# Optimization experiments

Hardware: AMD Instinct MI355X
Metric: run time of the kernel (lower is better)

The kernel has to match this reference:

```python
import jax, jax.numpy as jnp
import numpy as np

H = 2048   # hidden_size
NH = 32    # n_head
HS = 64    # head_size
B, T = 2, 4096
D_DECAY, D_AAA, D_MV, D_GATE = 96, 96, 64, 256


def setup_inputs() -> dict:
    key = jax.random.key(0)
    ks = jax.random.split(key, 30)
    rn = lambda k, s, sc=0.02: jax.random.normal(k, s, jnp.float32) * sc
    d = {}
    d['x'] = jax.random.normal(ks[0], (B, T, H), jnp.float32)
    d['shift_state_in'] = jax.random.normal(ks[1], (B, H), jnp.float32)
    d['wkv_state_in'] = jnp.zeros((B, NH, HS, HS), jnp.float32)
    d['v_first_val'] = jax.random.normal(ks[2], (B, T, H), jnp.float32)
    for i, n in enumerate(['x_r', 'x_w', 'x_k', 'x_v', 'x_a', 'x_g']):
        d[n] = jax.random.uniform(ks[3 + i], (H,), jnp.float32)
    d['w0'] = rn(ks[9], (H,)) - 4.0
    d['w1'] = rn(ks[10], (H, D_DECAY)); d['w2'] = rn(ks[11], (D_DECAY, H))
    d['a0'] = rn(ks[12], (H,)); d['a1'] = rn(ks[13], (H, D_AAA)); d['a2'] = rn(ks[14], (D_AAA, H))
    d['v0'] = rn(ks[15], (H,)) + 1.0; d['v1'] = rn(ks[16], (H, D_MV)); d['v2'] = rn(ks[17], (D_MV, H))
    d['g1'] = rn(ks[18], (H, D_GATE)); d['g2'] = rn(ks[19], (D_GATE, H))
    d['k_k'] = jnp.full((H,), 0.85, jnp.float32)
    d['k_a'] = jnp.ones((H,), jnp.float32)
    d['r_k'] = rn(ks[20], (NH, HS))
    s = 1.0 / np.sqrt(H)
    d['W_r'] = jax.random.normal(ks[21], (H, H), jnp.float32) * s
    d['W_k'] = jax.random.normal(ks[22], (H, H), jnp.float32) * s
    d['W_v'] = jax.random.normal(ks[23], (H, H), jnp.float32) * s
    d['W_o'] = jax.random.normal(ks[24], (H, H), jnp.float32) * s
    d['ln_w'] = jnp.ones((H,), jnp.float32)
    d['ln_b'] = jnp.zeros((H,), jnp.float32)
    return d


def _forward(x, shift_state_in, wkv_state_in, v_first_val, x_r, x_w, x_k, x_v, x_a, x_g,
             w0, w1, w2, a0, a1, a2, v0, v1, v2, g1, g2, k_k, k_a, r_k,
             W_r, W_k, W_v, W_o, ln_w, ln_b):
    Bx, Tx, C = x.shape
    # token shift: previous token embedding (shift_state for t=0)
    xprev = jnp.concatenate([shift_state_in[:, None, :], x[:, :-1]], axis=1)
    dx = xprev - x
    xr, xw, xk, xv, xa, xg = (x + dx * m for m in (x_r, x_w, x_k, x_v, x_a, x_g))
    r = xr @ W_r.T
    k = xk @ W_k.T
    v = xv @ W_v.T
    # soft-clamped log-decay (<= -0.5)
    w_raw = -jax.nn.softplus(-(w0 + jnp.tanh(xw @ w1) @ w2)) - 0.5
    # layer_id > 0: residual mix with first-layer value
    v = v + (v_first_val - v) * jax.nn.sigmoid(v0 + (xv @ v1) @ v2)
    a = jax.nn.sigmoid(a0 + (xa @ a1) @ a2)          # in-context learning rate
    g = jax.nn.sigmoid(xg @ g1) @ g2                 # output gate
    kk = (k * k_k).reshape(Bx, Tx, NH, HS)
    kk = kk / jnp.maximum(jnp.linalg.norm(kk, axis=-1, keepdims=True), 1e-12)  # F.normalize
    kk = kk.reshape(Bx, Tx, C)
    k = k * (1.0 + (a - 1.0) * k_a)
    w = jnp.exp(-jnp.exp(w_raw))                     # per-channel decay in (0,1)
    heads = lambda t: t.reshape(Bx, Tx, NH, HS).transpose(1, 0, 2, 3)  # [T,B,NH,HS]
    rs, ws, ks_, vs, kks, as_ = map(heads, (r, w, k, v, kk, a))

    def step(S, inp):
        # S: [B,NH,HS(value),HS(key)]
        rt, wt, kt, vt, kkt, at = inp
        sa = jnp.einsum('bhvk,bhk->bhv', S, -kkt)
        S = (S * wt[:, :, None, :]
             + sa[:, :, :, None] * (kkt * at)[:, :, None, :]
             + vt[:, :, :, None] * kt[:, :, None, :])
        return S, jnp.einsum('bhvk,bhk->bhv', S, rt)

    wkv_state_out, y = jax.lax.scan(step, wkv_state_in, (rs, ws, ks_, vs, kks, as_))
    y = y.transpose(1, 0, 2, 3)                      # [B,T,NH,HS]
    # GroupNorm(n_head groups, eps=1e-5*head_size)
    mu = y.mean(-1, keepdims=True)
    var = y.var(-1, keepdims=True)
    y = ((y - mu) / jnp.sqrt(var + 1e-5 * HS)).reshape(Bx, Tx, C) * ln_w + ln_b
    rk = (r.reshape(Bx, Tx, NH, HS) * k.reshape(Bx, Tx, NH, HS) * r_k).sum(-1, keepdims=True)
    y = y + (rk * v.reshape(Bx, Tx, NH, HS)).reshape(Bx, Tx, C)
    out = (y * g) @ W_o.T
    return out, x[:, -1], wkv_state_out, v_first_val


def reference(x, shift_state_in, wkv_state_in, v_first_val, x_r, x_w, x_k, x_v, x_a, x_g,
              w0, w1, w2, a0, a1, a2, v0, v1, v2, g1, g2, k_k, k_a, r_k,
              W_r, W_k, W_v, W_o, ln_w, ln_b):
    return _forward(x, shift_state_in, wkv_state_in, v_first_val, x_r, x_w, x_k, x_v, x_a, x_g,
                    w0, w1, w2, a0, a1, a2, v0, v1, v2, g1, g2, k_k, k_a, r_k,
                    W_r, W_k, W_v, W_o, ln_w, ln_b)
```

## Files before the change

### kernel.cpp

```cpp
#include <hip/hip_runtime.h>

typedef unsigned short u16;
typedef __attribute__((ext_vector_type(4))) float f32x4;
typedef __attribute__((ext_vector_type(8))) __bf16 bf16x8;
typedef __attribute__((ext_vector_type(8))) unsigned short u16x8;
typedef __attribute__((ext_vector_type(4))) unsigned short u16x4;

#define DI static __device__ __forceinline__

DI float bfu2f(u16 u){ unsigned int x = ((unsigned int)u)<<16; float f; __builtin_memcpy(&f,&x,4); return f; }
DI u16 f2bfu(float f){ __bf16 h = (__bf16)f; u16 u; __builtin_memcpy(&u,&h,2); return u; }
DI float sigm(float x){ return 1.f/(1.f+expf(-x)); }

DI void gload_lds16(const void* g, void* l) {
  __builtin_amdgcn_global_load_lds(
      (const __attribute__((address_space(1))) unsigned int*)g,
      (__attribute__((address_space(3))) unsigned int*)l, 16, 0, 0);
}

template<bool OBF16>
__global__ __launch_bounds__(256) void gemm128_k(
    const u16* __restrict__ A, const u16* __restrict__ Bt,
    void* __restrict__ Cp, int M, int N, int K)
{
  __shared__ alignas(16) u16 As[128*64];
  __shared__ alignas(16) u16 Bs[128*64];
  const int tid = threadIdx.x;
  const int wid = tid >> 6, lane = tid & 63;
  const int wm = wid >> 1, wn = wid & 1;
  const int l15 = lane & 15, q = lane >> 4;
  const int m0 = blockIdx.x * 128, n0 = blockIdx.y * 128;
  const int sr = (wid << 3) + (lane >> 3);
  const int sc = (lane & 7) << 3;
  f32x4 acc[4][4];
  #pragma unroll
  for (int i=0;i<4;i++)
    #pragma unroll
    for (int j=0;j<4;j++) acc[i][j] = f32x4{0.f,0.f,0.f,0.f};

  char* la = (char*)As + (size_t)wid*1024;
  char* lb = (char*)Bs + (size_t)wid*1024;
  for (int k0 = 0; k0 < K; k0 += 64) {
    const u16* ga = A  + (size_t)(m0 + sr)*K + k0 + sc;
    const u16* gb = Bt + (size_t)(n0 + sr)*K + k0 + sc;
    #pragma unroll
    for (int it = 0; it < 4; ++it) {
      gload_lds16(ga + (size_t)(32*it)*K, la + it*4096);
      gload_lds16(gb + (size_t)(32*it)*K, lb + it*4096);
    }
    __syncthreads();
    #pragma unroll
    for (int ks = 0; ks < 64; ks += 32) {
      bf16x8 af[4], bfv[4];
      #pragma unroll
      for (int i=0;i<4;i++) af[i]  = *(const bf16x8*)&As[(wm*64 + i*16 + l15)*64 + ks + q*8];
      #pragma unroll
      for (int j=0;j<4;j++) bfv[j] = *(const bf16x8*)&Bs[(wn*64 + j*16 + l15)*64 + ks + q*8];
      #pragma unroll
      for (int i=0;i<4;i++)
        #pragma unroll
        for (int j=0;j<4;j++)
          acc[i][j] = __builtin_amdgcn_mfma_f32_16x16x32_bf16(af[i], bfv[j], acc[i][j], 0, 0, 0);
    }
    __syncthreads();
  }
  #pragma unroll
  for (int i=0;i<4;i++)
    #pragma unroll
    for (int j=0;j<4;j++)
      #pragma unroll
      for (int rr=0;rr<4;rr++) {
        const int gm = m0 + wm*64 + i*16 + q*4 + rr;
        const int gn = n0 + wn*64 + j*16 + l15;
        const size_t o = (size_t)gm * (size_t)N + gn;
        if constexpr (OBF16) ((u16*)Cp)[o] = f2bfu(acc[i][j][rr]);
        else                 ((float*)Cp)[o] = acc[i][j][rr];
      }
}

constexpr int LDW = 72;

template<bool MIX, bool WNK, bool ABF16, bool OBF16, int EPI=0>
__global__ __launch_bounds__(256) void gemm_k(
    const void* __restrict__ Ap, const float* __restrict__ dxp, const float* __restrict__ mixp,
    const float* __restrict__ Wp, void* __restrict__ Cp, int M, int N, int K)
{
  __shared__ alignas(16) __bf16 As[64*LDW];
  __shared__ alignas(16) __bf16 Bs[64*LDW];
  const int tid = threadIdx.x;
  const int m0 = blockIdx.x * 64;
  const int n0 = blockIdx.y * 64;
  const int lane = tid & 63, wid = tid >> 6;
  const int wm = wid >> 1, wn = wid & 1;
  const int l15 = lane & 15, q = lane >> 4;
  f32x4 acc[2][2] = {{{0.f,0.f,0.f,0.f},{0.f,0.f,0.f,0.f}},
                     {{0.f,0.f,0.f,0.f},{0.f,0.f,0.f,0.f}}};

  for (int k0 = 0; k0 < K; k0 += 64) {
    {
      const int kc = (tid & 7) * 8;
      const int r0 = tid >> 3;
      #pragma unroll
      for (int it = 0; it < 2; ++it) {
        const int row = r0 + 32*it;
        const size_t gmK = (size_t)(m0 + row) * (size_t)K;
        const int gk = k0 + kc;
        if constexpr (ABF16) {
          const u16* A16 = (const u16*)Ap;
          u16x8 u;
          if (gk + 7 < K) u = *(const u16x8*)(A16 + gmK + gk);
          else {
            #pragma unroll
            for (int e=0;e<8;e++) u[e] = (gk+e < K) ? A16[gmK + gk + e] : (u16)0;
          }
          *(u16x8*)&As[row*LDW + kc] = u;
        } else {
          const float* A32 = (const float*)Ap;
          float f[8];
          if (gk + 7 < K) {
            f32x4 va = *(const f32x4*)(A32 + gmK + gk);
            f32x4 vb = *(const f32x4*)(A32 + gmK + gk + 4);
            if constexpr (MIX) {
              f32x4 d0 = *(const f32x4*)(dxp + gmK + gk);
              f32x4 d1 = *(const f32x4*)(dxp + gmK + gk + 4);
              f32x4 c0 = *(const f32x4*)(mixp + gk);
              f32x4 c1 = *(const f32x4*)(mixp + gk + 4);
              va = va + d0*c0; vb = vb + d1*c1;
            }
            #pragma unroll
            for (int e=0;e<4;e++){ f[e]=va[e]; f[4+e]=vb[e]; }
          } else {
            #pragma unroll
            for (int e=0;e<8;e++){
              const int kk2 = gk+e;
              float xv = 0.f;
              if (kk2 < K) {
                xv = A32[gmK + kk2];
                if constexpr (MIX) xv = fmaf(dxp[gmK+kk2], mixp[kk2], xv);
              }
              f[e] = xv;
            }
          }
          bf16x8 v8;
          #pragma unroll
          for (int e=0;e<8;e++) v8[e] = (__bf16)f[e];
          *(bf16x8*)&As[row*LDW + kc] = v8;
        }
      }
    }
    if constexpr (WNK) {
      const int kc = (tid & 7) * 8;
      const int r0 = tid >> 3;
      #pragma unroll
      for (int it = 0; it < 2; ++it) {
        const int row = r0 + 32*it;
        const int gn = n0 + row;
        const int gk = k0 + kc;
        float f[8];
        if (gn < N && gk + 7 < K) {
          const size_t o = (size_t)gn * (size_t)K + gk;
          f32x4 va = *(const f32x4*)(Wp + o);
          f32x4 vb = *(const f32x4*)(Wp + o + 4);
          #pragma unroll
          for (int e=0;e<4;e++){ f[e]=va[e]; f[4+e]=vb[e]; }
        } else {
          #pragma unroll
          for (int e=0;e<8;e++) f[e] = (gn < N && gk+e < K) ? Wp[(size_t)gn*K + gk + e] : 0.f;
        }
        bf16x8 v8;
        #pragma unroll
        for (int e=0;e<8;e++) v8[e] = (__bf16)f[e];
        *(bf16x8*)&Bs[row*LDW + kc] = v8;
      }
    } else {
      const int nc = (tid & 15) * 4;
      const int kr = tid >> 4;
      #pragma unroll
      for (int it = 0; it < 4; ++it) {
        const int kk = kr + 16*it;
        const int gk = k0 + kk;
        f32x4 v = {0.f,0.f,0.f,0.f};
        if (gk < K) {
          const int gn = n0 + nc;
          if (gn + 3 < N) v = *(const f32x4*)(Wp + (size_t)gk*N + gn);
          else {
            #pragma unroll
            for (int e=0;e<4;e++) if (gn+e < N) v[e] = Wp[(size_t)gk*N + gn + e];
          }
        }
        #pragma unroll
        for (int e=0;e<4;e++) Bs[(nc+e)*LDW + kk] = (__bf16)v[e];
      }
    }
    __syncthreads();
    #pragma unroll
    for (int ks = 0; ks < 64; ks += 32) {
      bf16x8 af[2], bfv[2];
      #pragma unroll
      for (int i=0;i<2;i++) af[i]  = *(const bf16x8*)&As[(wm*32 + i*16 + l15)*LDW + ks + q*8];
      #pragma unroll
      for (int i=0;i<2;i++) bfv[i] = *(const bf16x8*)&Bs[(wn*32 + i*16 + l15)*LDW + ks + q*8];
      #pragma unroll
      for (int i=0;i<2;i++)
        #pragma unroll
        for (int j=0;j<2;j++)
          acc[i][j] = __builtin_amdgcn_mfma_f32_16x16x32_bf16(af[i], bfv[j], acc[i][j], 0, 0, 0);
    }
    __syncthreads();
  }
  #pragma unroll
  for (int i=0;i<2;i++) {
    #pragma unroll
    for (int j=0;j<2;j++) {
      #pragma unroll
      for (int rr=0;rr<4;rr++) {
        const int gm = m0 + wm*32 + i*16 + q*4 + rr;
        const int gn = n0 + wn*32 + j*16 + l15;
        if (gn < N) {
          const size_t o = (size_t)gm * (size_t)N + gn;
          if constexpr (EPI == 1) {
            float* C = (float*)Cp;
            const float s = sigm(mixp[gn] + acc[i][j][rr]);
            const float vG = C[o];
            C[o] = vG + (dxp[o] - vG) * s;
          } else if constexpr (OBF16) {
            ((u16*)Cp)[o] = f2bfu(acc[i][j][rr]);
          } else {
            ((float*)Cp)[o] = acc[i][j][rr];
          }
        }
      }
    }
  }
}

__global__ void mix_cast_k(const float* __restrict__ x, const float* __restrict__ shift,
    const float* __restrict__ mr, const float* __restrict__ mw, const float* __restrict__ mk,
    const float* __restrict__ mv, const float* __restrict__ ma, const float* __restrict__ mg,
    u16* __restrict__ xr_b, u16* __restrict__ xw_b, u16* __restrict__ xk_b,
    u16* __restrict__ xv_b, u16* __restrict__ xa_b, u16* __restrict__ xg_b,
    float* __restrict__ xlast, int T_, int B_)
{
  const int Hh = 2048;
  size_t e4 = (size_t)blockIdx.x*blockDim.x + threadIdx.x;
  size_t total4 = (size_t)B_*T_*Hh/4;
  if (e4 >= total4) return;
  size_t e = e4*4;
  size_t th = (size_t)T_*Hh;
  size_t b = e / th; size_t rem = e - b*th;
  int t = (int)(rem / Hh); int c = (int)(rem & (Hh-1));
  f32x4 xv4 = *(const f32x4*)(x+e);
  f32x4 xp = t ? *(const f32x4*)(x+e-Hh) : *(const f32x4*)(shift + b*Hh + c);
  f32x4 dx = xp - xv4;
  if (t == T_-1) *(f32x4*)(xlast + b*Hh + c) = xv4;
  #define EMIT(mp, dst) { \
    f32x4 mc = *(const f32x4*)(mp + c); \
    f32x4 r_ = xv4 + dx*mc; \
    u16x4 o_; \
    o_[0]=f2bfu(r_[0]); o_[1]=f2bfu(r_[1]); o_[2]=f2bfu(r_[2]); o_[3]=f2bfu(r_[3]); \
    *(u16x4*)(dst + e) = o_; }
  EMIT(mr, xr_b) EMIT(mw, xw_b) EMIT(mk, xk_b)
  EMIT(mv, xv_b) EMIT(ma, xa_b) EMIT(mg, xg_b)
  #undef EMIT
}

__global__ void castw_k(const float* __restrict__ src, u16* __restrict__ dst, long n4){
  long i = (long)blockIdx.x*blockDim.x + threadIdx.x;
  if (i < n4) {
    f32x4 v = ((const f32x4*)src)[i];
    u16x4 o; o[0]=f2bfu(v[0]); o[1]=f2bfu(v[1]); o[2]=f2bfu(v[2]); o[3]=f2bfu(v[3]);
    ((u16x4*)dst)[i] = o;
  }
}

__global__ void ew_tanh_k(u16* p, long n){
  long i = (long)blockIdx.x*blockDim.x + threadIdx.x;
  if (i < n) p[i] = f2bfu(tanhf(bfu2f(p[i])));
}
__global__ void ew_sig_k(u16* p, long n){
  long i = (long)blockIdx.x*blockDim.x + threadIdx.x;
  if (i < n) p[i] = f2bfu(sigm(bfu2f(p[i])));
}
__global__ void ew_w_k(float* p, const float* __restrict__ w0, long n){
  long i = (long)blockIdx.x*blockDim.x + threadIdx.x;
  if (i < n) {
    int c = (int)(i & 2047);
    float z = -(w0[c] + p[i]);
    float sp = (z > 20.f) ? z : log1pf(expf(z));
    p[i] = expf(-expf(-sp - 0.5f));
  }
}
__global__ void ew_a_k(u16* p, const float* __restrict__ a0, long n){
  long i = (long)blockIdx.x*blockDim.x + threadIdx.x;
  if (i < n) { int c = (int)(i & 2047); p[i] = f2bfu(sigm(a0[c] + bfu2f(p[i]))); }
}
__global__ void copy4_k(float* __restrict__ dst, const float* __restrict__ src, long n4){
  long i = (long)blockIdx.x*blockDim.x + threadIdx.x;
  if (i < n4) ((f32x4*)dst)[i] = ((const f32x4*)src)[i];
}

__global__ __launch_bounds__(256) void rnorm_k(
    const u16* __restrict__ kb, const float* __restrict__ kkw, float* __restrict__ r2)
{
  const size_t bt = blockIdx.x;
  const int tid = threadIdx.x;
  const int c0 = tid << 3;
  u16x8 kv8 = *(const u16x8*)(kb + bt*2048 + c0);
  f32x4 ka_ = *(const f32x4*)(kkw + c0);
  f32x4 kb_ = *(const f32x4*)(kkw + c0 + 4);
  float s = 0.f;
  #pragma unroll
  for (int e=0;e<4;e++){ float kk = bfu2f(kv8[e])*ka_[e];   s = fmaf(kk,kk,s); }
  #pragma unroll
  for (int e=0;e<4;e++){ float kk = bfu2f(kv8[4+e])*kb_[e]; s = fmaf(kk,kk,s); }
  s += __shfl_xor(s, 1, 64);
  s += __shfl_xor(s, 2, 64);
  s += __shfl_xor(s, 4, 64);
  if ((tid & 7) == 0) r2[bt*32 + (tid>>3)] = 1.f/fmaxf(s, 1e-24f);
}

__global__ __launch_bounds__(64) __attribute__((amdgpu_waves_per_eu(1, 4)))
void scan_k(
    const u16* __restrict__ rb, const float* __restrict__ wb, const u16* __restrict__ kb,
    const float* __restrict__ vb, const u16* __restrict__ ab,
    const float* __restrict__ kkw, const float* __restrict__ kaw,
    const float* __restrict__ S0, float* __restrict__ yb, float* __restrict__ Sout, int T_)
{
  const int Hh = 2048, NHl = 32;
  const int blk = blockIdx.x;
  const int b = blk >> 5, h = blk & 31;
  const int lane = threadIdx.x;
  float S[64];
  const size_t sbase = (((size_t)b*NHl + h)*64 + lane)*64;
  #pragma unroll
  for (int i=0;i<64;i++) S[i] = S0[sbase+i];
  const float kkc = kkw[h*64+lane], kac = kaw[h*64+lane];
  __shared__ alignas(16) float lw[64], lkk[64], lka[64], lke[64], lr[64];
  size_t idx = (size_t)b*T_*Hh + (size_t)h*64 + lane;
  float rv = bfu2f(rb[idx]), wv = wb[idx], kv = bfu2f(kb[idx]), vv = vb[idx], av = bfu2f(ab[idx]);
  for (int t=0; t<T_; ++t) {
    float kk = kv * kkc;
    float ssum = kk*kk;
    #pragma unroll
    for (int m=1;m<64;m<<=1) ssum += __shfl_xor(ssum, m, 64);
    float inv = 1.f / fmaxf(sqrtf(ssum), 1e-12f);
    float kkn = kk * inv;
    float ke  = kv * (1.f + (av - 1.f)*kac);
    lw[lane]=wv; lkk[lane]=kkn; lka[lane]=kkn*av; lke[lane]=ke; lr[lane]=rv;
    const float vt = vv;
    __syncthreads();
    float nrv=0.f,nwv=0.f,nkv=0.f,nvv=0.f,nav=0.f;
    if (t+1 < T_) {
      const size_t ni = idx + Hh;
      nrv = bfu2f(rb[ni]); nwv = wb[ni]; nkv = bfu2f(kb[ni]); nvv = vb[ni]; nav = bfu2f(ab[ni]);
    }
    const f32x4* KK4 = (const f32x4*)lkk;
    const f32x4* W4  = (const f32x4*)lw;
    const f32x4* KA4 = (const f32x4*)lka;
    const f32x4* KE4 = (const f32x4*)lke;
    const f32x4* R4  = (const f32x4*)lr;
    float sa0=0.f,sa1=0.f,sa2=0.f,sa3=0.f;
    #pragma unroll
    for (int qq=0;qq<16;qq++){
      f32x4 k4 = KK4[qq];
      sa0 = fmaf(S[4*qq+0], k4[0], sa0);
      sa1 = fmaf(S[4*qq+1], k4[1], sa1);
      sa2 = fmaf(S[4*qq+2], k4[2], sa2);
      sa3 = fmaf(S[4*qq+3], k4[3], sa3);
    }
    const float sa = -((sa0+sa1)+(sa2+sa3));
    float y0=0.f,y1=0.f,y2=0.f,y3=0.f;
    #pragma unroll
    for (int qq=0;qq<16;qq++){
      f32x4 w4=W4[qq], a4=KA4[qq], e4=KE4[qq], r4=R4[qq];
      float s_;
      s_ = fmaf(vt, e4[0], fmaf(sa, a4[0], S[4*qq+0]*w4[0])); S[4*qq+0]=s_; y0 = fmaf(s_, r4[0], y0);
      s_ = fmaf(vt, e4[1], fmaf(sa, a4[1], S[4*qq+1]*w4[1])); S[4*qq+1]=s_; y1 = fmaf(s_, r4[1], y1);
      s_ = fmaf(vt, e4[2], fmaf(sa, a4[2], S[4*qq+2]*w4[2])); S[4*qq+2]=s_; y2 = fmaf(s_, r4[2], y2);
      s_ = fmaf(vt, e4[3], fmaf(sa, a4[3], S[4*qq+3]*w4[3])); S[4*qq+3]=s_; y3 = fmaf(s_, r4[3], y3);
    }
    yb[idx] = (y0+y1)+(y2+y3);
    __syncthreads();
    rv=nrv; wv=nwv; kv=nkv; vv=nvv; av=nav;
    idx += Hh;
  }
  #pragma unroll
  for (int i=0;i<64;i++) Sout[sbase+i] = S[i];
}

__global__ __launch_bounds__(64) void chunk_mu_k(
    const u16* __restrict__ rb, const float* __restrict__ wb, const u16* __restrict__ kb,
    const float* __restrict__ vb, const u16* __restrict__ ab,
    const float* __restrict__ kkw, const float* __restrict__ kaw,
    const float* __restrict__ r2b,
    float* __restrict__ Mbuf, float* __restrict__ Ubuf, float* __restrict__ Dbuf,
    float* __restrict__ yb, int T_, int NC)
{
  const int ch = blockIdx.x;
  const int c  = ch % NC;
  const int bh = ch / NC;
  const int b = bh >> 5, h = bh & 31;
  const int lane = threadIdx.x;

  float SM[64], SU[64];
  #pragma unroll
  for (int i=0;i<64;i++) { SM[i] = (lane == i) ? 1.f : 0.f; SU[i] = 0.f; }

  const int hc = h*64 + lane;
  const float kkc = kkw[hc], kac = kaw[hc];

  __shared__ alignas(16) float LB[2][5][64];

  size_t idx = ((size_t)b*T_ + (size_t)c*64)*2048 + hc;
  size_t r2i = ((size_t)b*T_ + (size_t)c*64)*32 + h;
  float* dD = Dbuf + (size_t)ch*4096 + lane;

  {
    const float kv = bfu2f(kb[idx]);
    const float av = bfu2f(ab[idx]);
    const float kk = kv*kkc;
    LB[0][0][lane] = wb[idx];
    LB[0][1][lane] = kk;
    LB[0][2][lane] = kk*av;
    LB[0][3][lane] = kv*(1.f+(av-1.f)*kac);
    LB[0][4][lane] = bfu2f(rb[idx]);
  }
  float vv = vb[idx];
  float r2 = r2b[r2i];
  __syncthreads();

  for (int j=0; j<64; ++j) {
    const int cur = j & 1;
    float nr=0.f,nk=0.f,nw=0.f,na=0.f,nv=0.f,nr2=0.f;
    if (j+1 < 64) {
      const size_t ni = idx + 2048;
      nr = bfu2f(rb[ni]); nk = bfu2f(kb[ni]); nw = wb[ni]; na = bfu2f(ab[ni]); nv = vb[ni];
      nr2 = r2b[r2i + 32];
    }
    const f32x4* W4  = (const f32x4*)LB[cur][0];
    const f32x4* KK4 = (const f32x4*)LB[cur][1];
    const f32x4* KA4 = (const f32x4*)LB[cur][2];
    const f32x4* KE4 = (const f32x4*)LB[cur][3];
    const f32x4* R4  = (const f32x4*)LB[cur][4];
    float m0=0.f,m1=0.f,m2=0.f,m3=0.f;
    float u0=0.f,u1=0.f,u2=0.f,u3=0.f;
    #pragma unroll
    for (int qq=0;qq<16;qq++){
      f32x4 k4 = KK4[qq];
      m0 = fmaf(SM[4*qq+0], k4[0], m0);
      m1 = fmaf(SM[4*qq+1], k4[1], m1);
      m2 = fmaf(SM[4*qq+2], k4[2], m2);
      m3 = fmaf(SM[4*qq+3], k4[3], m3);
      u0 = fmaf(SU[4*qq+0], k4[0], u0);
      u1 = fmaf(SU[4*qq+1], k4[1], u1);
      u2 = fmaf(SU[4*qq+2], k4[2], u2);
      u3 = fmaf(SU[4*qq+3], k4[3], u3);
    }
    const float saM = -((m0+m1)+(m2+m3)) * r2;
    const float saU = -((u0+u1)+(u2+u3)) * r2;
    const float vt = vv;
    float d0=0.f,d1=0.f,d2=0.f,d3=0.f;
    float y0=0.f,y1=0.f,y2=0.f,y3=0.f;
    #pragma unroll
    for (int qq=0;qq<16;qq++){
      f32x4 w4=W4[qq], a4=KA4[qq], e4=KE4[qq], r4=R4[qq];
      float s_;
      s_ = fmaf(saM, a4[0], SM[4*qq+0]*w4[0]); SM[4*qq+0]=s_; d0 = fmaf(s_, r4[0], d0);
      s_ = fmaf(saM, a4[1], SM[4*qq+1]*w4[1]); SM[4*qq+1]=s_; d1 = fmaf(s_, r4[1], d1);
      s_ = fmaf(saM, a4[2], SM[4*qq+2]*w4[2]); SM[4*qq+2]=s_; d2 = fmaf(s_, r4[2], d2);
      s_ = fmaf(saM, a4[3], SM[4*qq+3]*w4[3]); SM[4*qq+3]=s_; d3 = fmaf(s_, r4[3], d3);
      s_ = fmaf(vt, e4[0], fmaf(saU, a4[0], SU[4*qq+0]*w4[0])); SU[4*qq+0]=s_; y0 = fmaf(s_, r4[0], y0);
      s_ = fmaf(vt, e4[1], fmaf(saU, a4[1], SU[4*qq+1]*w4[1])); SU[4*qq+1]=s_; y1 = fmaf(s_, r4[1], y1);
      s_ = fmaf(vt, e4[2], fmaf(saU, a4[2], SU[4*qq+2]*w4[2])); SU[4*qq+2]=s_; y2 = fmaf(s_, r4[2], y2);
      s_ = fmaf(vt, e4[3], fmaf(saU, a4[3], SU[4*qq+3]*w4[3])); SU[4*qq+3]=s_; y3 = fmaf(s_, r4[3], y3);
    }
    dD[(size_t)j*64] = (d0+d1)+(d2+d3);
    yb[idx] = (y0+y1)+(y2+y3);
    if (j+1 < 64) {
      const float kk = nk*kkc;
      LB[cur^1][0][lane] = nw;
      LB[cur^1][1][lane] = kk;
      LB[cur^1][2][lane] = kk*na;
      LB[cur^1][3][lane] = nk*(1.f+(na-1.f)*kac);
      LB[cur^1][4][lane] = nr;
    }
    __syncthreads();
    vv = nv; r2 = nr2;
    idx += 2048; r2i += 32;
  }
  float* md = Mbuf + (size_t)ch*4096 + (size_t)lane*64;
  float* ud = Ubuf + (size_t)ch*4096 + (size_t)lane*64;
  #pragma unroll
  for (int qq=0;qq<16;qq++){
    *(f32x4*)(md + 4*qq) = f32x4{SM[4*qq+0],SM[4*qq+1],SM[4*qq+2],SM[4*qq+3]};
    *(f32x4*)(ud + 4*qq) = f32x4{SU[4*qq+0],SU[4*qq+1],SU[4*qq+2],SU[4*qq+3]};
  }
}

__global__ __launch_bounds__(256) void propagate_k(
    const float* __restrict__ Mbuf, const float* Ubuf,
    const float* __restrict__ S0, float* SSbuf, float* __restrict__ Sout, int NC)
{
  const int bh   = blockIdx.x >> 2;
  const int v0r  = (blockIdx.x & 3) * 16;
  const int tid  = threadIdx.x;
  const int lane = tid & 63;
  const int wvv  = tid >> 6;

  __shared__ float MT[64*65];
  __shared__ float Srow[16][64];

  #pragma unroll
  for (int i=0;i<4;i++) {
    const int v = v0r + wvv*4 + i;
    Srow[wvv*4+i][lane] = S0[((size_t)bh*64 + v)*64 + lane];
  }

  const size_t mbase = (size_t)bh * NC * 4096;
  f32x4 mreg[4];
  #pragma unroll
  for (int it=0; it<4; ++it)
    mreg[it] = *(const f32x4*)(Mbuf + mbase + it*1024 + tid*4);

  for (int c=0; c<NC; ++c) {
    const size_t chB = mbase + (size_t)c*4096;
    #pragma unroll
    for (int it=0; it<4; ++it) {
      const int base = it*1024 + tid*4;
      const int j = base >> 6;
      const int k = base & 63;
      #pragma unroll
      for (int e=0;e<4;e++) MT[(k+e)*65 + j] = mreg[it][e];
    }
    __syncthreads();
    if (c+1 < NC) {
      #pragma unroll
      for (int it=0; it<4; ++it)
        mreg[it] = *(const f32x4*)(Mbuf + chB + 4096 + it*1024 + tid*4);
    }
    float u[4];
    #pragma unroll
    for (int i=0;i<4;i++)
      u[i] = Ubuf[chB + (size_t)(v0r + wvv*4 + i)*64 + lane];
    #pragma unroll
    for (int i=0;i<4;i++)
      SSbuf[chB + (size_t)(v0r + wvv*4 + i)*64 + lane] = Srow[wvv*4+i][lane];
    float acc[4] = {0.f,0.f,0.f,0.f};
    #pragma unroll
    for (int j4=0; j4<16; ++j4) {
      float m0_ = MT[lane*65 + j4*4 + 0];
      float m1_ = MT[lane*65 + j4*4 + 1];
      float m2_ = MT[lane*65 + j4*4 + 2];
      float m3_ = MT[lane*65 + j4*4 + 3];
      #pragma unroll
      for (int i=0;i<4;i++) {
        f32x4 s4 = *(const f32x4*)&Srow[wvv*4+i][j4*4];
        acc[i] = fmaf(s4[0], m0_, acc[i]);
        acc[i] = fmaf(s4[1], m1_, acc[i]);
        acc[i] = fmaf(s4[2], m2_, acc[i]);
        acc[i] = fmaf(s4[3], m3_, acc[i]);
      }
    }
    #pragma unroll
    for (int i=0;i<4;i++) Srow[wvv*4+i][lane] = acc[i] + u[i];
    __syncthreads();
  }
  #pragma unroll
  for (int i=0;i<4;i++) {
    const int v = v0r + wvv*4 + i;
    Sout[((size_t)bh*64 + v)*64 + lane] = Srow[wvv*4+i][lane];
  }
}

__global__ __launch_bounds__(64) void ycorr_k(
    const float* __restrict__ SSbuf, const float* __restrict__ Dbuf,
    float* __restrict__ yb, int T_, int NC)
{
  const int ch = blockIdx.x;
  const int c  = ch % NC;
  const int bh = ch / NC;
  const int b = bh >> 5, h = bh & 31;
  const int lane = threadIdx.x;

  __shared__ alignas(16) float Dl[64*68];

  {
    const float* sg = SSbuf + (size_t)ch*4096;
    #pragma unroll
    for (int i=0;i<16;i++){
      const int o = i*256 + lane*4;
      f32x4 v = *(const f32x4*)(sg + o);
      *(f32x4*)&Dl[(o>>6)*68 + (o&63)] = v;
    }
  }
  __syncthreads();
  float ss[64];
  #pragma unroll
  for (int qq=0;qq<16;qq++){
    f32x4 v = *(const f32x4*)&Dl[lane*68 + 4*qq];
    ss[4*qq+0]=v[0]; ss[4*qq+1]=v[1]; ss[4*qq+2]=v[2]; ss[4*qq+3]=v[3];
  }
  __syncthreads();
  {
    const float* dg = Dbuf + (size_t)ch*4096;
    #pragma unroll
    for (int i=0;i<16;i++){
      const int o = i*256 + lane*4;
      f32x4 v = *(const f32x4*)(dg + o);
      *(f32x4*)&Dl[(o>>6)*68 + (o&63)] = v;
    }
  }
  __syncthreads();

  size_t idx = ((size_t)b*T_ + (size_t)c*64)*2048 + (size_t)h*64 + lane;
  for (int t=0; t<64; ++t) {
    const f32x4* D4 = (const f32x4*)&Dl[t*68];
    float a0=0.f,a1=0.f,a2=0.f,a3=0.f;
    #pragma unroll
    for (int qq=0;qq<16;qq++){
      f32x4 d4 = D4[qq];
      a0 = fmaf(ss[4*qq+0], d4[0], a0);
      a1 = fmaf(ss[4*qq+1], d4[1], a1);
      a2 = fmaf(ss[4*qq+2], d4[2], a2);
      a3 = fmaf(ss[4*qq+3], d4[3], a3);
    }
    yb[idx] = yb[idx] + ((a0+a1)+(a2+a3));
    idx += 2048;
  }
}

__global__ __launch_bounds__(256) void post_k(
    const float* __restrict__ yb, const u16* __restrict__ rb, const u16* __restrict__ kb,
    const u16* __restrict__ ab, const u16* __restrict__ gb, const float* __restrict__ vb,
    const float* __restrict__ kaw, const float* __restrict__ rkw,
    const float* __restrict__ lnw, const float* __restrict__ lnb, u16* __restrict__ zb)
{
  const int wid = threadIdx.x >> 6, lane = threadIdx.x & 63;
  const size_t unit = (size_t)blockIdx.x*4 + wid;
  const size_t bt = unit >> 5; const int h = (int)(unit & 31);
  const size_t idx = bt*2048 + (size_t)h*64 + lane;
  const int hc = h*64 + lane;
  const float yv = yb[idx];
  const float rv = bfu2f(rb[idx]), kv = bfu2f(kb[idx]), av = bfu2f(ab[idx]);
  const float ke = kv*(1.f + (av-1.f)*kaw[hc]);
  float s1 = yv, s2 = yv*yv, rk = rv*ke*rkw[hc];
  #pragma unroll
  for (int m=1;m<64;m<<=1){
    s1 += __shfl_xor(s1,m,64);
    s2 += __shfl_xor(s2,m,64);
    rk += __shfl_xor(rk,m,64);
  }
  const float mean = s1 * (1.f/64.f);
  const float var  = s2 * (1.f/64.f) - mean*mean;
  const float rstd = rsqrtf(var + 6.4e-4f);
  const float zn = (yv-mean)*rstd*lnw[hc] + lnb[hc] + rk*vb[idx];
  zb[idx] = f2bfu(zn * bfu2f(gb[idx]));
}

extern "C" void kernel_launch(void* const* d_in, const int* in_sizes, int n_in,
                              void* d_out, int out_size, void* d_ws, size_t ws_size,
                              hipStream_t stream)
{
  const float* x      = (const float*)d_in[0];
  const float* shift  = (const float*)d_in[1];
  const float* wkv0   = (const float*)d_in[2];
  const float* vfirst = (const float*)d_in[3];
  const float* xr = (const float*)d_in[4];
  const float* xw = (const float*)d_in[5];
  const float* xk = (const float*)d_in[6];
  const float* xv = (const float*)d_in[7];
  const float* xa = (const float*)d_in[8];
  const float* xg = (const float*)d_in[9];
  const float* w0 = (const float*)d_in[10];
  const float* w1 = (const float*)d_in[11];
  const float* w2 = (const float*)d_in[12];
  const float* a0 = (const float*)d_in[13];
  const float* a1 = (const float*)d_in[14];
  const float* a2 = (const float*)d_in[15];
  const float* v0 = (const float*)d_in[16];
  const float* v1 = (const float*)d_in[17];
  const float* v2 = (const float*)d_in[18];
  const float* g1 = (const float*)d_in[19];
  const float* g2 = (const float*)d_in[20];
  const float* k_k = (const float*)d_in[21];
  const float* k_a = (const float*)d_in[22];
  const float* r_k = (const float*)d_in[23];
  const float* W_r = (const float*)d_in[24];
  const float* W_k = (const float*)d_in[25];
  const float* W_v = (const float*)d_in[26];
  const float* W_o = (const float*)d_in[27];
  const float* ln_w = (const float*)d_in[28];
  const float* ln_b = (const float*)d_in[29];

  const int H = 2048, NH = 32;
  const int BH = in_sizes[1];
  const int B  = BH / H;
  const long BTH = (long)in_sizes[0];
  const int T  = (int)(BTH / BH);
  const int M  = (int)(BTH / H);

  float* out0 = (float*)d_out;
  float* out1 = out0 + BTH;
  float* out2 = out1 + BH;
  float* out3 = out2 + (size_t)B*NH*64*64;

  char* ws = (char*)d_ws;
  u16* mixb = (u16*)ws;  ws += (size_t)BTH*12;
  u16* xr_b = mixb + 0*BTH;
  u16* xw_b = mixb + 1*BTH;
  u16* xk_b = mixb + 2*BTH;
  u16* xv_b = mixb + 3*BTH;
  u16* xa_b = mixb + 4*BTH;
  u16* xg_b = mixb + 5*BTH;
  float* Mbuf  = (float*)mixb;
  float* Ubuf  = Mbuf + BTH;
  float* Dbuf  = Ubuf + BTH;
  float* SSbuf = Ubuf;
  u16*   zb16  = (u16*)mixb;
  u16* rb   = (u16*)ws;  ws += BTH*2;
  u16* kb   = (u16*)ws;  ws += BTH*2;
  u16* ab   = (u16*)ws;  ws += BTH*2;
  u16* gb   = (u16*)ws;  ws += BTH*2;
  u16* wr16 = (u16*)ws;  ws += (size_t)H*H*2;
  u16* wk16 = (u16*)ws;  ws += (size_t)H*H*2;
  u16* wv16 = (u16*)ws;  ws += (size_t)H*H*2;
  u16* wo16 = (u16*)ws;  ws += (size_t)H*H*2;
  u16* h1w  = (u16*)ws;  ws += (size_t)M*96*2;
  u16* h1a  = (u16*)ws;  ws += (size_t)M*96*2;
  u16* h1v  = (u16*)ws;  ws += (size_t)M*64*2;
  u16* h1g  = (u16*)ws;  ws += (size_t)M*256*2;
  float* dxz = (float*)ws; ws += BTH*4;
  float* r2b = (float*)h1w;
  const size_t ws_need = (size_t)(ws - (char*)d_ws);
  const bool chunked = (ws_size >= ws_need) && (T % 64 == 0);
  const bool big_ok  = (M % 128 == 0);
  (void)n_in; (void)out_size;

  const dim3 blk(256);
  auto gg  = [&](int N){ return dim3(M/64, (N+63)/64); };
  auto gg128 = [&](int N){ return dim3(M/128, N/128); };

  mix_cast_k<<<dim3((unsigned)((BTH/4 + 255)/256)), blk, 0, stream>>>(
      x, shift, xr, xw, xk, xv, xa, xg, xr_b, xw_b, xk_b, xv_b, xa_b, xg_b, out1, T, B);

  {
    const long n4 = (long)H*H/4;
    const dim3 gw((unsigned)((n4 + 255)/256));
    castw_k<<<gw, blk, 0, stream>>>(W_r, wr16, n4);
    castw_k<<<gw, blk, 0, stream>>>(W_k, wk16, n4);
    castw_k<<<gw, blk, 0, stream>>>(W_v, wv16, n4);
    castw_k<<<gw, blk, 0, stream>>>(W_o, wo16, n4);
  }

  gemm_k<false,false,true,true><<<gg(96),  blk, 0, stream>>>(xw_b, nullptr, nullptr, w1, h1w, M, 96,  H);
  gemm_k<false,false,true,true><<<gg(96),  blk, 0, stream>>>(xa_b, nullptr, nullptr, a1, h1a, M, 96,  H);
  gemm_k<false,false,true,true><<<gg(64),  blk, 0, stream>>>(xv_b, nullptr, nullptr, v1, h1v, M, 64,  H);
  gemm_k<false,false,true,true><<<gg(256), blk, 0, stream>>>(xg_b, nullptr, nullptr, g1, h1g, M, 256, H);

  ew_tanh_k<<<dim3((unsigned)(((long)M*96 + 255)/256)),  blk, 0, stream>>>(h1w, (long)M*96);
  ew_sig_k <<<dim3((unsigned)(((long)M*256 + 255)/256)), blk, 0, stream>>>(h1g, (long)M*256);

  if (big_ok) {
    gemm128_k<true ><<<gg128(H), blk, 0, stream>>>(xr_b, wr16, rb,   M, H, H);
    gemm128_k<true ><<<gg128(H), blk, 0, stream>>>(xk_b, wk16, kb,   M, H, H);
    gemm128_k<false><<<gg128(H), blk, 0, stream>>>(xv_b, wv16, out3, M, H, H);
  } else {
    gemm_k<false,true,true,true ><<<gg(H), blk, 0, stream>>>(xr_b, nullptr, nullptr, W_r, rb,   M, H, H);
    gemm_k<false,true,true,true ><<<gg(H), blk, 0, stream>>>(xk_b, nullptr, nullptr, W_k, kb,   M, H, H);
    gemm_k<false,true,true,false><<<gg(H), blk, 0, stream>>>(xv_b, nullptr, nullptr, W_v, out3, M, H, H);
  }

  gemm_k<false,false,true,false  ><<<gg(H), blk, 0, stream>>>(h1w, nullptr, nullptr, w2, dxz, M, H, 96);
  rnorm_k<<<dim3((unsigned)M), blk, 0, stream>>>(kb, k_k, r2b);
  gemm_k<false,false,true,true   ><<<gg(H), blk, 0, stream>>>(h1a, nullptr, nullptr, a2, ab,  M, H, 96);
  gemm_k<false,false,true,false,1><<<gg(H), blk, 0, stream>>>(h1v, vfirst,  v0,      v2, out3, M, H, 64);
  gemm_k<false,false,true,true   ><<<gg(H), blk, 0, stream>>>(h1g, nullptr, nullptr, g2, gb,  M, H, 256);

  const unsigned nbB = (unsigned)((BTH + 255)/256);
  ew_w_k<<<dim3(nbB), blk, 0, stream>>>(dxz, w0, BTH);
  ew_a_k<<<dim3(nbB), blk, 0, stream>>>(ab, a0, BTH);

  if (chunked) {
    const int NC = T / 64;
    const int CH = B * NH * NC;
    chunk_mu_k <<<dim3(CH),     dim3(64),  0, stream>>>(rb, dxz, kb, out3, ab, k_k, k_a, r2b,
                                                        Mbuf, Ubuf, Dbuf, out0, T, NC);
    propagate_k<<<dim3(B*NH*4), blk,       0, stream>>>(Mbuf, Ubuf, wkv0, SSbuf, out2, NC);
    ycorr_k    <<<dim3(CH),     dim3(64),  0, stream>>>(SSbuf, Dbuf, out0, T, NC);
  } else {
    scan_k<<<dim3(B*NH), dim3(64), 0, stream>>>(rb, dxz, kb, out3, ab, k_k, k_a, wkv0, out0, out2, T);
  }

  post_k<<<dim3((unsigned)((size_t)M*NH/4)), blk, 0, stream>>>(out0, rb, kb, ab, gb, out3,
                                                               k_a, r_k, ln_w, ln_b, zb16);

  copy4_k<<<dim3((unsigned)((BTH/4 + 255)/256)), blk, 0, stream>>>(out3, vfirst, BTH/4);

  if (big_ok) {
    gemm128_k<false><<<gg128(H), blk, 0, stream>>>(zb16, wo16, out0, M, H, H);
  } else {
    gemm_k<false,true,true,false><<<gg(H), blk, 0, stream>>>(zb16, nullptr, nullptr, W_o, out0, M, H, H);
  }
}
```

Measured before the change: 2.209 ms.

## Split chunk scan M and U state updates across separate wavefronts

The per-chunk WKV kernel previously had each 64-lane wavefront carry two 64-float state rows (the transition matrix M and the input-driven U) in registers. Now each chunk is handled by two wavefronts, one per role, packed four wavefronts to a 256-thread block. Each wavefront keeps its own LDS double buffer, so no block barrier is needed. This halves per-thread register pressure and doubles the number of parallel waves, at the cost of loading and preprocessing the r/k/w/a inputs twice per chunk.

Result: faster. 1.956 ms (-11.5%).

```diff
diff --git a/kernel.cpp b/kernel.cpp
--- a/kernel.cpp
+++ b/kernel.cpp
@@ -388,7 +388,7 @@
   for (int i=0;i<64;i++) Sout[sbase+i] = S[i];
 }
 
-__global__ __launch_bounds__(64) void chunk_mu_k(
+__global__ __launch_bounds__(256) void chunk_mu_k(
     const u16* __restrict__ rb, const float* __restrict__ wb, const u16* __restrict__ kb,
     const float* __restrict__ vb, const u16* __restrict__ ab,
     const float* __restrict__ kkw, const float* __restrict__ kaw,
@@ -396,20 +396,24 @@
     float* __restrict__ Mbuf, float* __restrict__ Ubuf, float* __restrict__ Dbuf,
     float* __restrict__ yb, int T_, int NC)
 {
-  const int ch = blockIdx.x;
+  const int wid  = threadIdx.x >> 6;
+  const int lane = threadIdx.x & 63;
+  const int g    = blockIdx.x * 4 + wid;
+  const int ch   = g >> 1;
+  const bool mrole = ((g & 1) == 0);
   const int c  = ch % NC;
   const int bh = ch / NC;
   const int b = bh >> 5, h = bh & 31;
-  const int lane = threadIdx.x;
-
-  float SM[64], SU[64];
-  #pragma unroll
-  for (int i=0;i<64;i++) { SM[i] = (lane == i) ? 1.f : 0.f; SU[i] = 0.f; }
+
+  float S[64];
+  #pragma unroll
+  for (int i=0;i<64;i++) S[i] = (mrole && lane == i) ? 1.f : 0.f;
 
   const int hc = h*64 + lane;
   const float kkc = kkw[hc], kac = kaw[hc];
 
-  __shared__ alignas(16) float LB[2][5][64];
+  __shared__ alignas(16) float LB[4][2][5][64];
+  float (*Lw)[5][64] = LB[wid];
 
   size_t idx = ((size_t)b*T_ + (size_t)c*64)*2048 + hc;
   size_t r2i = ((size_t)b*T_ + (size_t)c*64)*32 + h;
@@ -419,82 +423,79 @@
     const float kv = bfu2f(kb[idx]);
     const float av = bfu2f(ab[idx]);
     const float kk = kv*kkc;
-    LB[0][0][lane] = wb[idx];
-    LB[0][1][lane] = kk;
-    LB[0][2][lane] = kk*av;
-    LB[0][3][lane] = kv*(1.f+(av-1.f)*kac);
-    LB[0][4][lane] = bfu2f(rb[idx]);
-  }
-  float vv = vb[idx];
+    Lw[0][0][lane] = wb[idx];
+    Lw[0][1][lane] = kk;
+    Lw[0][2][lane] = kk*av;
+    Lw[0][3][lane] = kv*(1.f+(av-1.f)*kac);
+    Lw[0][4][lane] = bfu2f(rb[idx]);
+  }
+  float vv = mrole ? 0.f : vb[idx];
   float r2 = r2b[r2i];
-  __syncthreads();
 
   for (int j=0; j<64; ++j) {
     const int cur = j & 1;
     float nr=0.f,nk=0.f,nw=0.f,na=0.f,nv=0.f,nr2=0.f;
     if (j+1 < 64) {
       const size_t ni = idx + 2048;
-      nr = bfu2f(rb[ni]); nk = bfu2f(kb[ni]); nw = wb[ni]; na = bfu2f(ab[ni]); nv = vb[ni];
+      nr = bfu2f(rb[ni]); nk = bfu2f(kb[ni]); nw = wb[ni]; na = bfu2f(ab[ni]);
+      if (!mrole) nv = vb[ni];
       nr2 = r2b[r2i + 32];
     }
-    const f32x4* W4  = (const f32x4*)LB[cur][0];
-    const f32x4* KK4 = (const f32x4*)LB[cur][1];
-    const f32x4* KA4 = (const f32x4*)LB[cur][2];
-    const f32x4* KE4 = (const f32x4*)LB[cur][3];
-    const f32x4* R4  = (const f32x4*)LB[cur][4];
-    float m0=0.f,m1=0.f,m2=0.f,m3=0.f;
-    float u0=0.f,u1=0.f,u2=0.f,u3=0.f;
+    const f32x4* W4  = (const f32x4*)Lw[cur][0];
+    const f32x4* KK4 = (const f32x4*)Lw[cur][1];
+    const f32x4* KA4 = (const f32x4*)Lw[cur][2];
+    const f32x4* KE4 = (const f32x4*)Lw[cur][3];
+    const f32x4* R4  = (const f32x4*)Lw[cur][4];
+    float s0=0.f,s1=0.f,s2=0.f,s3=0.f;
     #pragma unroll
     for (int qq=0;qq<16;qq++){
       f32x4 k4 = KK4[qq];
-      m0 = fmaf(SM[4*qq+0], k4[0], m0);
-      m1 = fmaf(SM[4*qq+1], k4[1], m1);
-      m2 = fmaf(SM[4*qq+2], k4[2], m2);
-      m3 = fmaf(SM[4*qq+3], k4[3], m3);
-      u0 = fmaf(SU[4*qq+0], k4[0], u0);
-      u1 = fmaf(SU[4*qq+1], k4[1], u1);
-      u2 = fmaf(SU[4*qq+2], k4[2], u2);
-      u3 = fmaf(SU[4*qq+3], k4[3], u3);
-    }
-    const float saM = -((m0+m1)+(m2+m3)) * r2;
-    const float saU = -((u0+u1)+(u2+u3)) * r2;
+      s0 = fmaf(S[4*qq+0], k4[0], s0);
+      s1 = fmaf(S[4*qq+1], k4[1], s1);
+      s2 = fmaf(S[4*qq+2], k4[2], s2);
+      s3 = fmaf(S[4*qq+3], k4[3], s3);
+    }
+    const float sa = -((s0+s1)+(s2+s3)) * r2;
     const float vt = vv;
-    float d0=0.f,d1=0.f,d2=0.f,d3=0.f;
     float y0=0.f,y1=0.f,y2=0.f,y3=0.f;
-    #pragma unroll
-    for (int qq=0;qq<16;qq++){
-      f32x4 w4=W4[qq], a4=KA4[qq], e4=KE4[qq], r4=R4[qq];
-      float s_;
-      s_ = fmaf(saM, a4[0], SM[4*qq+0]*w4[0]); SM[4*qq+0]=s_; d0 = fmaf(s_, r4[0], d0);
-      s_ = fmaf(saM, a4[1], SM[4*qq+1]*w4[1]); SM[4*qq+1]=s_; d1 = fmaf(s_, r4[1], d1);
-      s_ = fmaf(saM, a4[2], SM[4*qq+2]*w4[2]); SM[4*qq+2]=s_; d2 = fmaf(s_, r4[2], d2);
-      s_ = fmaf(saM, a4[3], SM[4*qq+3]*w4[3]); SM[4*qq+3]=s_; d3 = fmaf(s_, r4[3], d3);
-      s_ = fmaf(vt, e4[0], fmaf(saU, a4[0], SU[4*qq+0]*w4[0])); SU[4*qq+0]=s_; y0 = fmaf(s_, r4[0], y0);
-      s_ = fmaf(vt, e4[1], fmaf(saU, a4[1], SU[4*qq+1]*w4[1])); SU[4*qq+1]=s_; y1 = fmaf(s_, r4[1], y1);
-      s_ = fmaf(vt, e4[2], fmaf(saU, a4[2], SU[4*qq+2]*w4[2])); SU[4*qq+2]=s_; y2 = fmaf(s_, r4[2], y2);
-      s_ = fmaf(vt, e4[3], fmaf(saU, a4[3], SU[4*qq+3]*w4[3])); SU[4*qq+3]=s_; y3 = fmaf(s_, r4[3], y3);
-    }
-    dD[(size_t)j*64] = (d0+d1)+(d2+d3);
-    yb[idx] = (y0+y1)+(y2+y3);
+    if (mrole) {
+      #pragma unroll
+      for (int qq=0;qq<16;qq++){
+        f32x4 w4=W4[qq], a4=KA4[qq], r4=R4[qq];
+        float s_;
+        s_ = fmaf(sa, a4[0], S[4*qq+0]*w4[0]); S[4*qq+0]=s_; y0 = fmaf(s_, r4[0], y0);
+        s_ = fmaf(sa, a4[1], S[4*qq+1]*w4[1]); S[4*qq+1]=s_; y1 = fmaf(s_, r4[1], y1);
+        s_ = fmaf(sa, a4[2], S[4*qq+2]*w4[2]); S[4*qq+2]=s_; y2 = fmaf(s_, r4[2], y2);
+        s_ = fmaf(sa, a4[3], S[4*qq+3]*w4[3]); S[4*qq+3]=s_; y3 = fmaf(s_, r4[3], y3);
+      }
+      dD[(size_t)j*64] = (y0+y1)+(y2+y3);
+    } else {
+      #pragma unroll
+      for (int qq=0;qq<16;qq++){
+        f32x4 w4=W4[qq], a4=KA4[qq], e4=KE4[qq], r4=R4[qq];
+        float s_;
+        s_ = fmaf(vt, e4[0], fmaf(sa, a4[0], S[4*qq+0]*w4[0])); S[4*qq+0]=s_; y0 = fmaf(s_, r4[0], y0);
+        s_ = fmaf(vt, e4[1], fmaf(sa, a4[1], S[4*qq+1]*w4[1])); S[4*qq+1]=s_; y1 = fmaf(s_, r4[1], y1);
+        s_ = fmaf(vt, e4[2], fmaf(sa, a4[2], S[4*qq+2]*w4[2])); S[4*qq+2]=s_; y2 = fmaf(s_, r4[2], y2);
+        s_ = fmaf(vt, e4[3], fmaf(sa, a4[3], S[4*qq+3]*w4[3])); S[4*qq+3]=s_; y3 = fmaf(s_, r4[3], y3);
+      }
+      yb[idx] = (y0+y1)+(y2+y3);
+    }
     if (j+1 < 64) {
       const float kk = nk*kkc;
-      LB[cur^1][0][lane] = nw;
-      LB[cur^1][1][lane] = kk;
-      LB[cur^1][2][lane] = kk*na;
-      LB[cur^1][3][lane] = nk*(1.f+(na-1.f)*kac);
-      LB[cur^1][4][lane] = nr;
-    }
-    __syncthreads();
+      Lw[cur^1][0][lane] = nw;
+      Lw[cur^1][1][lane] = kk;
+      Lw[cur^1][2][lane] = kk*na;
+      Lw[cur^1][3][lane] = nk*(1.f+(na-1.f)*kac);
+      Lw[cur^1][4][lane] = nr;
+    }
     vv = nv; r2 = nr2;
     idx += 2048; r2i += 32;
   }
-  float* md = Mbuf + (size_t)ch*4096 + (size_t)lane*64;
-  float* ud = Ubuf + (size_t)ch*4096 + (size_t)lane*64;
-  #pragma unroll
-  for (int qq=0;qq<16;qq++){
-    *(f32x4*)(md + 4*qq) = f32x4{SM[4*qq+0],SM[4*qq+1],SM[4*qq+2],SM[4*qq+3]};
-    *(f32x4*)(ud + 4*qq) = f32x4{SU[4*qq+0],SU[4*qq+1],SU[4*qq+2],SU[4*qq+3]};
-  }
+  float* fd = (mrole ? Mbuf : Ubuf) + (size_t)ch*4096 + (size_t)lane*64;
+  #pragma unroll
+  for (int qq=0;qq<16;qq++)
+    *(f32x4*)(fd + 4*qq) = f32x4{S[4*qq+0],S[4*qq+1],S[4*qq+2],S[4*qq+3]};
 }
 
 __global__ __launch_bounds__(256) void propagate_k(
@@ -783,8 +784,8 @@
   if (chunked) {
     const int NC = T / 64;
     const int CH = B * NH * NC;
-    chunk_mu_k <<<dim3(CH),     dim3(64),  0, stream>>>(rb, dxz, kb, out3, ab, k_k, k_a, r2b,
-                                                        Mbuf, Ubuf, Dbuf, out0, T, NC);
+    chunk_mu_k <<<dim3((unsigned)(2*CH/4)), blk, 0, stream>>>(rb, dxz, kb, out3, ab, k_k, k_a, r2b,
+                                                              Mbuf, Ubuf, Dbuf, out0, T, NC);
     propagate_k<<<dim3(B*NH*4), blk,       0, stream>>>(Mbuf, Ubuf, wkv0, SSbuf, out2, NC);
     ycorr_k    <<<dim3(CH),     dim3(64),  0, stream>>>(SSbuf, Dbuf, out0, T, NC);
   } else {
```
